# Kernel tuning notes

Hardware: AMD Instinct MI355X
Metric: run time of the kernel (lower is better)

## Reference

```python
import jax, jax.numpy as jnp
import numpy as np

EPS = 1e-12


def _pchip_slopes(y, x):
    """PCHIP (Fritsch-Carlson) slopes. y: (S, K), x: (K) -> (S, K)."""
    K = y.shape[-1]
    if K < 2:
        return jnp.zeros_like(y)
    h = x[1:] - x[:-1]                              # (K-1,)
    delta = (y[..., 1:] - y[..., :-1]) / (h + EPS)  # (S, K-1)
    if K == 2:
        return jnp.broadcast_to(delta[..., :1], y.shape).astype(y.dtype)
    # interior slopes: weighted harmonic mean where secants agree in sign
    delta_prev = delta[..., :-1]
    delta_next = delta[..., 1:]
    same_sign = delta_prev * delta_next > 0
    h_prev = h[:-1]
    h_next = h[1:]
    w1 = 2.0 * h_next + h_prev
    w2 = h_next + 2.0 * h_prev
    denom = w1 / (delta_prev + EPS) + w2 / (delta_next + EPS)
    d_int = (w1 + w2) / (denom + EPS)
    d_mid = jnp.where(same_sign, d_int, jnp.zeros_like(d_int))  # (S, K-2)
    # left endpoint (one-sided, shape-limited)
    h0, h1 = h[0], h[1]
    delta0 = delta[..., 0]
    delta1 = delta[..., 1]
    d0 = ((2.0 * h0 + h1) * delta0 - h0 * delta1) / (h0 + h1 + EPS)
    d0 = jnp.where(jnp.sign(d0) != jnp.sign(delta0), jnp.zeros_like(d0), d0)
    d0 = jnp.where((jnp.sign(delta0) != jnp.sign(delta1)) & (jnp.abs(d0) > 3.0 * jnp.abs(delta0)), 3.0 * delta0, d0)
    # right endpoint
    hn1, hn2 = h[-1], h[-2]
    deltan1 = delta[..., -1]
    deltan2 = delta[..., -2]
    dn = ((2.0 * hn1 + hn2) * deltan1 - hn1 * deltan2) / (hn1 + hn2 + EPS)
    dn = jnp.where(jnp.sign(dn) != jnp.sign(deltan1), jnp.zeros_like(dn), dn)
    dn = jnp.where((jnp.sign(deltan1) != jnp.sign(deltan2)) & (jnp.abs(dn) > 3.0 * jnp.abs(deltan1)), 3.0 * deltan1, dn)
    return jnp.concatenate([d0[..., None], d_mid, dn[..., None]], axis=-1)


def setup_inputs() -> dict:
    key = jax.random.key(0)
    k1, k2 = jax.random.split(key)
    B, S, K = 4096, 4096, 64
    x_min, x_max = -3.0, 3.0
    xq = jax.random.normal(k1, (B, S), dtype=jnp.float32) * 2.0  # some queries outside domain
    coeffs = jax.random.normal(k2, (S, K), dtype=jnp.float32)
    knots = jnp.linspace(x_min, x_max, K, dtype=jnp.float32)
    return {"xq": xq, "coeffs": coeffs, "knots": knots}


def reference(xq, coeffs, knots):
    y = coeffs                                   # (S, K)
    d = _pchip_slopes(y, knots)                  # (S, K)
    K = knots.shape[0]
    x0_dom = knots[0]
    x1_dom = knots[-1]
    below = xq < x0_dom
    above = xq > x1_dom
    xq_c = jnp.clip(xq, x0_dom, x1_dom)
    idx = jnp.searchsorted(knots, xq_c) - 1      # (B, S) interval index
    idx = jnp.clip(idx, 0, K - 2)
    x0 = knots[idx]
    x1 = knots[idx + 1]
    h = x1 - x0 + EPS
    t = (xq_c - x0) / h
    t2 = t * t
    t3 = t2 * t
    h00 = 2.0 * t3 - 3.0 * t2 + 1.0
    h10 = t3 - 2.0 * t2 + t
    h01 = -2.0 * t3 + 3.0 * t2
    h11 = t3 - t2
    s_idx = jnp.arange(y.shape[0])[None, :]      # (1, S) spline index
    y0 = y[s_idx, idx]
    y1 = y[s_idx, idx + 1]
    d0 = d[s_idx, idx]
    d1 = d[s_idx, idx + 1]
    interp = h00 * y0 + h10 * h * d0 + h01 * y1 + h11 * h * d1
    out = jnp.where(below, y[None, :, 0] + d[None, :, 0] * (xq - x0_dom), interp)
    out = jnp.where(above, y[None, :, -1] + d[None, :, -1] * (xq - x1_dom), out)
    return out
```

## Files before the change

### kernel.cpp

```cpp
#include <hip/hip_runtime.h>

#define EPSF 1e-12f
#define STILE 64
#define KK 64
#define LSTR 65

__device__ __forceinline__ float sgnf(float x) {
    return (x > 0.f) ? 1.f : ((x < 0.f) ? -1.f : 0.f);
}

__global__ __launch_bounds__(256) void pchip_fused(
    const float* __restrict__ xq,
    const float* __restrict__ coeffs,
    const float* __restrict__ knots,
    float* __restrict__ out,
    int S, int b_chunk)
{
    __shared__ float yp[STILE * LSTR];
    __shared__ float dpl[STILE * LSTR];
    __shared__ float skn[KK];

    int tid = threadIdx.x;
    int s0 = blockIdx.x * STILE;
    int b0 = blockIdx.y * b_chunk;

    if (tid < KK) skn[tid] = knots[tid];
    for (int t = tid; t < STILE * KK; t += 256) {
        int sl = t >> 6, k = t & 63;
        yp[sl * LSTR + k] = coeffs[(size_t)(s0 + sl) * KK + k];
    }
    __syncthreads();
    for (int t = tid; t < STILE * KK; t += 256) {
        int sl = t >> 6, k = t & 63;
        if (k < KK - 1) {
            float h = skn[k + 1] - skn[k];
            dpl[sl * LSTR + k] = (yp[sl * LSTR + k + 1] - yp[sl * LSTR + k]) / (h + EPSF);
        }
    }
    __syncthreads();
    float dreg[16];
#pragma unroll
    for (int i = 0; i < 16; i++) {
        int t = tid + i * 256;
        int sl = t >> 6, k = t & 63;
        const float* del = dpl + sl * LSTR;
        float d;
        if (k == 0) {
            float h0 = skn[1] - skn[0], h1 = skn[2] - skn[1];
            float de0 = del[0], de1 = del[1];
            d = ((2.f * h0 + h1) * de0 - h0 * de1) / (h0 + h1 + EPSF);
            if (sgnf(d) != sgnf(de0)) d = 0.f;
            if ((sgnf(de0) != sgnf(de1)) && (fabsf(d) > 3.f * fabsf(de0))) d = 3.f * de0;
        } else if (k == KK - 1) {
            float hn1 = skn[KK - 1] - skn[KK - 2], hn2 = skn[KK - 2] - skn[KK - 3];
            float dn1 = del[KK - 2], dn2 = del[KK - 3];
            d = ((2.f * hn1 + hn2) * dn1 - hn1 * dn2) / (hn1 + hn2 + EPSF);
            if (sgnf(d) != sgnf(dn1)) d = 0.f;
            if ((sgnf(dn1) != sgnf(dn2)) && (fabsf(d) > 3.f * fabsf(dn1))) d = 3.f * dn1;
        } else {
            float dprev = del[k - 1], dnext = del[k];
            float hp = skn[k] - skn[k - 1], hn = skn[k + 1] - skn[k];
            bool same = dprev * dnext > 0.f;
            float w1 = 2.f * hn + hp;
            float w2 = hn + 2.f * hp;
            float denom = w1 / (dprev + EPSF) + w2 / (dnext + EPSF);
            float dint = (w1 + w2) / (denom + EPSF);
            d = same ? dint : 0.f;
        }
        dreg[i] = d;
    }
    __syncthreads();
#pragma unroll
    for (int i = 0; i < 16; i++) {
        int t = tid + i * 256;
        int sl = t >> 6, k = t & 63;
        dpl[sl * LSTR + k] = dreg[i];
    }
    __syncthreads();

    float x0d = skn[0], x1d = skn[KK - 1];
    float invh = (float)(KK - 1) / (x1d - x0d);
    float huni = 1.0f / invh + EPSF;
    int wave = tid >> 6, lane = tid & 63;
    const float* yrow = yp + lane * LSTR;
    const float* drow = dpl + lane * LSTR;

    int rows_per_wave = b_chunk >> 2;
    int base = b0 + wave * rows_per_wave;
    for (int ii = 0; ii < rows_per_wave; ii += 4) {
        size_t off0 = (size_t)(base + ii) * S + s0 + lane;
        float xv[4];
#pragma unroll
        for (int j = 0; j < 4; j++) xv[j] = xq[off0 + (size_t)j * S];
        float rv[4];
#pragma unroll
        for (int j = 0; j < 4; j++) {
            float x = xv[j];
            float xc = fminf(fmaxf(x, x0d), x1d);
            float tf = (xc - x0d) * invh;
            int idx = min((int)tf, KK - 2);
            float t = tf - (float)idx;
            float y0 = yrow[idx], y1 = yrow[idx + 1];
            float d0 = drow[idx], d1 = drow[idx + 1];
            float t2 = t * t, t3 = t2 * t;
            float h00 = 2.f * t3 - 3.f * t2 + 1.f;
            float h10 = t3 - 2.f * t2 + t;
            float h01 = -2.f * t3 + 3.f * t2;
            float h11 = t3 - t2;
            float res = h00 * y0 + h10 * huni * d0 + h01 * y1 + h11 * huni * d1;
            if (x < x0d) res = y0 + d0 * (x - x0d);
            if (x > x1d) res = y1 + d1 * (x - x1d);
            rv[j] = res;
        }
#pragma unroll
        for (int j = 0; j < 4; j++) out[off0 + (size_t)j * S] = rv[j];
    }
}

extern "C" void kernel_launch(void* const* d_in, const int* in_sizes, int n_in,
                              void* d_out, int out_size, void* d_ws, size_t ws_size,
                              hipStream_t stream) {
    const float* xq     = (const float*)d_in[0];
    const float* coeffs = (const float*)d_in[1];
    const float* knots  = (const float*)d_in[2];
    float* out = (float*)d_out;

    int K = in_sizes[2];
    int S = in_sizes[1] / K;
    int N = in_sizes[0];
    int B = N / S;

    int n_btiles = 16;
    int b_chunk = B / n_btiles;
    dim3 grid(S / STILE, n_btiles);
    pchip_fused<<<grid, 256, 0, stream>>>(xq, coeffs, knots, out, S, b_chunk);
}
```

Baseline: 136.9 us.

## Precompute per-interval cubic polynomial coefficients and enlarge blocks with deeper unroll

Each interval's Hermite form is converted into monomial cubic coefficients (c0..c3) held in four shared-memory planes. Each query then needs one Horner evaluation plus a derivative-based linear extrapolation, which removes the basis-function arithmetic and the below/above branches. The block grows to 512 threads with 8-row unroll and half as many batch tiles, aiming for more loads in flight. In exchange, shared memory per block roughly doubles and the set-up phase gains an extra pass, which could lower occupancy; the kernel is memory bound, so the arithmetic savings may not matter much.

```diff
diff --git a/kernel.cpp b/kernel.cpp
--- a/kernel.cpp
+++ b/kernel.cpp
@@ -4,46 +4,57 @@
 #define STILE 64
 #define KK 64
 #define LSTR 65
+#define PLANE (STILE * LSTR)
+#define BLK 512
+#define UNROLL 8
 
 __device__ __forceinline__ float sgnf(float x) {
     return (x > 0.f) ? 1.f : ((x < 0.f) ? -1.f : 0.f);
 }
 
-__global__ __launch_bounds__(256) void pchip_fused(
+__global__ __launch_bounds__(BLK, 4) void pchip_fused2(
     const float* __restrict__ xq,
     const float* __restrict__ coeffs,
     const float* __restrict__ knots,
     float* __restrict__ out,
     int S, int b_chunk)
 {
-    __shared__ float yp[STILE * LSTR];
-    __shared__ float dpl[STILE * LSTR];
+    __shared__ float pl[4 * PLANE];
     __shared__ float skn[KK];
 
     int tid = threadIdx.x;
     int s0 = blockIdx.x * STILE;
     int b0 = blockIdx.y * b_chunk;
 
+    float* p0 = pl;
+    float* p1 = pl + PLANE;
+    float* p2 = pl + 2 * PLANE;
+    float* p3 = pl + 3 * PLANE;
+
     if (tid < KK) skn[tid] = knots[tid];
-    for (int t = tid; t < STILE * KK; t += 256) {
-        int sl = t >> 6, k = t & 63;
-        yp[sl * LSTR + k] = coeffs[(size_t)(s0 + sl) * KK + k];
+#pragma unroll
+    for (int i = 0; i < (STILE * KK) / BLK; i++) {
+        int p = tid + i * BLK;
+        int sl = p >> 6, k = p & 63;
+        p0[sl * LSTR + k] = coeffs[(size_t)(s0 + sl) * KK + k];
     }
     __syncthreads();
-    for (int t = tid; t < STILE * KK; t += 256) {
-        int sl = t >> 6, k = t & 63;
+#pragma unroll
+    for (int i = 0; i < (STILE * KK) / BLK; i++) {
+        int p = tid + i * BLK;
+        int sl = p >> 6, k = p & 63;
         if (k < KK - 1) {
             float h = skn[k + 1] - skn[k];
-            dpl[sl * LSTR + k] = (yp[sl * LSTR + k + 1] - yp[sl * LSTR + k]) / (h + EPSF);
+            p3[sl * LSTR + k] = (p0[sl * LSTR + k + 1] - p0[sl * LSTR + k]) / (h + EPSF);
         }
     }
     __syncthreads();
-    float dreg[16];
+    float dreg[(STILE * KK) / BLK];
 #pragma unroll
-    for (int i = 0; i < 16; i++) {
-        int t = tid + i * 256;
-        int sl = t >> 6, k = t & 63;
-        const float* del = dpl + sl * LSTR;
+    for (int i = 0; i < (STILE * KK) / BLK; i++) {
+        int p = tid + i * BLK;
+        int sl = p >> 6, k = p & 63;
+        const float* del = p3 + sl * LSTR;
         float d;
         if (k == 0) {
             float h0 = skn[1] - skn[0], h1 = skn[2] - skn[1];
@@ -71,49 +82,73 @@
     }
     __syncthreads();
 #pragma unroll
-    for (int i = 0; i < 16; i++) {
-        int t = tid + i * 256;
-        int sl = t >> 6, k = t & 63;
-        dpl[sl * LSTR + k] = dreg[i];
+    for (int i = 0; i < (STILE * KK) / BLK; i++) {
+        int p = tid + i * BLK;
+        int sl = p >> 6, k = p & 63;
+        p2[sl * LSTR + k] = dreg[i];
+    }
+    __syncthreads();
+    float c1r[(STILE * KK) / BLK], c2r[(STILE * KK) / BLK], c3r[(STILE * KK) / BLK];
+#pragma unroll
+    for (int i = 0; i < (STILE * KK) / BLK; i++) {
+        int p = tid + i * BLK;
+        int sl = p >> 6, k = p & 63;
+        int kc = min(k, KK - 2);
+        int ib = sl * LSTR + kc;
+        float y0 = p0[ib], y1 = p0[ib + 1];
+        float d0 = p2[ib], d1 = p2[ib + 1];
+        float h = skn[kc + 1] - skn[kc] + EPSF;
+        c1r[i] = h * d0;
+        c2r[i] = 3.f * (y1 - y0) - h * (2.f * d0 + d1);
+        c3r[i] = 2.f * (y0 - y1) + h * (d0 + d1);
+    }
+    __syncthreads();
+#pragma unroll
+    for (int i = 0; i < (STILE * KK) / BLK; i++) {
+        int p = tid + i * BLK;
+        int sl = p >> 6, k = p & 63;
+        if (k < KK - 1) {
+            int ib = sl * LSTR + k;
+            p1[ib] = c1r[i];
+            p2[ib] = c2r[i];
+            p3[ib] = c3r[i];
+        }
     }
     __syncthreads();
 
     float x0d = skn[0], x1d = skn[KK - 1];
     float invh = (float)(KK - 1) / (x1d - x0d);
-    float huni = 1.0f / invh + EPSF;
+    float af = invh, bf = -x0d * invh;
     int wave = tid >> 6, lane = tid & 63;
-    const float* yrow = yp + lane * LSTR;
-    const float* drow = dpl + lane * LSTR;
+    const float* q0 = p0 + lane * LSTR;
+    const float* q1 = p1 + lane * LSTR;
+    const float* q2 = p2 + lane * LSTR;
+    const float* q3 = p3 + lane * LSTR;
 
-    int rows_per_wave = b_chunk >> 2;
-    int base = b0 + wave * rows_per_wave;
-    for (int ii = 0; ii < rows_per_wave; ii += 4) {
-        size_t off0 = (size_t)(base + ii) * S + s0 + lane;
-        float xv[4];
+    int rows_per_wave = b_chunk >> 3;
+    size_t off0 = (size_t)(b0 + wave * rows_per_wave) * S + s0 + lane;
+    for (int ii = 0; ii < rows_per_wave; ii += UNROLL) {
+        float xv[UNROLL];
 #pragma unroll
-        for (int j = 0; j < 4; j++) xv[j] = xq[off0 + (size_t)j * S];
-        float rv[4];
+        for (int j = 0; j < UNROLL; j++) xv[j] = xq[off0 + (size_t)j * S];
+        float rv[UNROLL];
 #pragma unroll
-        for (int j = 0; j < 4; j++) {
+        for (int j = 0; j < UNROLL; j++) {
             float x = xv[j];
-            float xc = fminf(fmaxf(x, x0d), x1d);
-            float tf = (xc - x0d) * invh;
-            int idx = min((int)tf, KK - 2);
-            float t = tf - (float)idx;
-            float y0 = yrow[idx], y1 = yrow[idx + 1];
-            float d0 = drow[idx], d1 = drow[idx + 1];
-            float t2 = t * t, t3 = t2 * t;
-            float h00 = 2.f * t3 - 3.f * t2 + 1.f;
-            float h10 = t3 - 2.f * t2 + t;
-            float h01 = -2.f * t3 + 3.f * t2;
-            float h11 = t3 - t2;
-            float res = h00 * y0 + h10 * huni * d0 + h01 * y1 + h11 * huni * d1;
-            if (x < x0d) res = y0 + d0 * (x - x0d);
-            if (x > x1d) res = y1 + d1 * (x - x1d);
-            rv[j] = res;
+            float tf = fmaf(x, af, bf);
+            float tcf = fminf(fmaxf(tf, 0.f), (float)(KK - 1));
+            int idx = min((int)tcf, KK - 2);
+            float t = tcf - (float)idx;
+            float c0 = q0[idx], c1 = q1[idx], c2 = q2[idx], c3 = q3[idx];
+            float P = fmaf(fmaf(fmaf(c3, t, c2), t, c1), t, c0);
+            float w = fmaf(fmaf(t, 2.f, t), c3, c2 + c2);
+            float Pp = fmaf(t, w, c1);
+            float ext = tf - tcf;
+            rv[j] = fmaf(Pp, ext, P);
         }
 #pragma unroll
-        for (int j = 0; j < 4; j++) out[off0 + (size_t)j * S] = rv[j];
+        for (int j = 0; j < UNROLL; j++) out[off0 + (size_t)j * S] = rv[j];
+        off0 += (size_t)UNROLL * S;
     }
 }
 
@@ -130,8 +165,8 @@
     int N = in_sizes[0];
     int B = N / S;
 
-    int n_btiles = 16;
+    int n_btiles = 8;
     int b_chunk = B / n_btiles;
     dim3 grid(S / STILE, n_btiles);
-    pchip_fused<<<grid, 256, 0, stream>>>(xq, coeffs, knots, out, S, b_chunk);
+    pchip_fused2<<<grid, BLK, 0, stream>>>(xq, coeffs, knots, out, S, b_chunk);
 }
```

Measured after the change: 123.9 us. 1.1x faster.
